# Kernel tuning notes

Hardware: AMD Instinct MI355X
Metric: run time of the kernel (lower is better)

## Reference

```python
import jax, jax.numpy as jnp
import numpy as np

EPS = 1e-12  # matches torch F.normalize eps


def _l2_normalize(x, axis):
    n = jnp.sqrt(jnp.sum(x * x, axis=axis, keepdims=True))
    return x / jnp.maximum(n, EPS)


def setup_inputs() -> dict:
    key = jax.random.key(0)
    k1, k2 = jax.random.split(key)
    phi = jax.random.normal(k1, (64, 512), dtype=jnp.float32)          # (m, H)
    psi = jax.random.normal(k2, (64, 1024, 512), dtype=jnp.float32)    # (m, n, W)
    return {"phi": phi, "psi": psi}


def reference(phi, psi):
    phi = phi.astype(jnp.float32)
    psi = psi.astype(jnp.float32)
    m, H = phi.shape
    m2, n, W = psi.shape
    phi = _l2_normalize(phi, axis=1)   # rows of phi
    psi = _l2_normalize(psi, axis=2)   # each measurement vector

    g_phi_sq = jnp.square(phi @ phi.T)  # (m, m)

    # b[i, j] = sum_{u,v} (psi[i,u] . psi[j,v])^2 = ||psi_i psi_j^T||_F^2
    #         = <psi_i^T psi_i, psi_j^T psi_j>_F  (exact identity, avoids (m,m,n,n))
    S = jnp.einsum('inw,inv->iwv', psi, psi)   # (m, W, W) per-block Gram
    b = jnp.einsum('iwv,jwv->ij', S, S)        # (m, m)

    loss = jnp.sum(g_phi_sq * b) - jnp.float32(m * n)
    return loss
```

## Files before the change

### kernel.cpp

```cpp
#include <hip/hip_runtime.h>
#include <hip/hip_bf16.h>

typedef unsigned short u16;
typedef unsigned int u32;
typedef __attribute__((ext_vector_type(8))) short short8x;
typedef __attribute__((ext_vector_type(4))) float f32x4;

__device__ __forceinline__ u16 bf16u(float x) {
    __hip_bfloat16 h = __float2bfloat16(x);
    return *reinterpret_cast<u16*>(&h);
}

__device__ __forceinline__ void gload_lds16(const void* g, void* l) {
    __builtin_amdgcn_global_load_lds(
        (const __attribute__((address_space(1))) u32*)g,
        (__attribute__((address_space(3))) u32*)l, 16, 0, 0);
}

#define M_  64
#define N_  1024
#define W_  512
#define SP_ROW 163840

__global__ __launch_bounds__(256) void psinorm_t(const float* __restrict__ psi,
                                                 const float* __restrict__ phi,
                                                 u16* __restrict__ psiT,
                                                 float* __restrict__ g2,
                                                 float* __restrict__ out) {
    const int t = threadIdx.x;
    __shared__ u32 tile[64][257];
    __shared__ float djs[4][64], nsqs[64];

    if (blockIdx.x < 1024) {
        const int i  = blockIdx.x >> 4;
        const int nb = blockIdx.x & 15;
        const float* base = psi + ((size_t)i * N_ + (size_t)nb * 64) * W_;
        const int sub = t & 15;

#pragma unroll
        for (int pp = 0; pp < 4; ++pp) {
            const int r = pp * 16 + (t >> 4);
            const float4* rb = (const float4*)(base + (size_t)r * W_) + sub;
            float4 v[8];
            float s = 0.f;
#pragma unroll
            for (int k = 0; k < 8; ++k) {
                v[k] = rb[k * 16];
                s += v[k].x * v[k].x + v[k].y * v[k].y + v[k].z * v[k].z + v[k].w * v[k].w;
            }
#pragma unroll
            for (int o = 1; o < 16; o <<= 1) s += __shfl_xor(s, o);
            const float inv = 1.0f / fmaxf(sqrtf(s), 1e-12f);
#pragma unroll
            for (int k = 0; k < 8; ++k) {
                u32 p0 = (u32)bf16u(v[k].x * inv) | ((u32)bf16u(v[k].y * inv) << 16);
                u32 p1 = (u32)bf16u(v[k].z * inv) | ((u32)bf16u(v[k].w * inv) << 16);
                const int wh = sub * 2 + k * 32;
                tile[r][wh]     = p0;
                tile[r][wh + 1] = p1;
            }
        }
        __syncthreads();

        const u16* t16 = (const u16*)&tile[0][0];
        const int lane = t & 63, wv = t >> 6;
        const int q  = lane & 31;
        const int l5 = lane >> 5;
        u32* out32 = (u32*)psiT + (size_t)i * (W_ * N_ / 2) + nb * 32;
#pragma unroll 4
        for (int it = 0; it < 64; ++it) {
            const int w = it * 8 + wv * 2 + l5;
            u32 lo = (u32)t16[(2 * q)     * 514 + w];
            u32 hi = (u32)t16[(2 * q + 1) * 514 + w];
            out32[(size_t)w * 512 + q] = lo | (hi << 16);
        }
    } else {
        const int gb = blockIdx.x - 1024;
        const int i0 = gb * 4;
        const int lane = t & 63, wv = t >> 6;
        float* pis = (float*)&tile[0][0];
#pragma unroll
        for (int r = 0; r < 4; ++r) {
            pis[r * 512 + t]       = phi[(i0 + r) * 512 + t];
            pis[r * 512 + 256 + t] = phi[(i0 + r) * 512 + 256 + t];
        }
        __syncthreads();

        for (int jj = 0; jj < 16; ++jj) {
            int j = wv + jj * 4;
            const float* pj = phi + j * 512;
            float nn = 0.f, d0 = 0.f, d1 = 0.f, d2 = 0.f, d3 = 0.f;
#pragma unroll
            for (int e = 0; e < 8; ++e) {
                float x = pj[lane + e * 64];
                nn += x * x;
                d0 += pis[0 * 512 + lane + e * 64] * x;
                d1 += pis[1 * 512 + lane + e * 64] * x;
                d2 += pis[2 * 512 + lane + e * 64] * x;
                d3 += pis[3 * 512 + lane + e * 64] * x;
            }
#pragma unroll
            for (int o = 32; o; o >>= 1) {
                nn += __shfl_xor(nn, o);
                d0 += __shfl_xor(d0, o);
                d1 += __shfl_xor(d1, o);
                d2 += __shfl_xor(d2, o);
                d3 += __shfl_xor(d3, o);
            }
            if (lane == 0) {
                djs[0][j] = d0; djs[1][j] = d1; djs[2][j] = d2; djs[3][j] = d3;
                nsqs[j] = nn;
            }
        }
        __syncthreads();
        if (t < 64) {
            const int j = t;
            const float invj = 1.0f / fmaxf(sqrtf(nsqs[j]), 1e-12f);
#pragma unroll
            for (int r = 0; r < 4; ++r) {
                const float invi = 1.0f / fmaxf(sqrtf(nsqs[i0 + r]), 1e-12f);
                const float g = djs[r][j] * invi * invj;
                g2[(i0 + r) * 64 + j] = g * g;
            }
        }
        if (gb == 0 && t == 0) out[0] = -65536.0f;
    }
}

__global__ __launch_bounds__(256) void syrk_bf16(const u16* __restrict__ psiT,
                                                 u16* __restrict__ Sp) {
    const int L = blockIdx.x;
    const int q = L >> 3;
    const int i  = (L & 7) * 8 + q / 10;
    const int bt = q % 10;
    int tr, tc;
    if      (bt < 4) { tr = 0; tc = bt;     }
    else if (bt < 7) { tr = 1; tc = bt - 3; }
    else if (bt < 9) { tr = 2; tc = bt - 5; }
    else             { tr = 3; tc = 3;      }
    const int t = threadIdx.x;

    const u16* Abase = psiT + (size_t)i * W_ * N_ + (size_t)tr * 128 * N_;
    const u16* Bbase = psiT + (size_t)i * W_ * N_ + (size_t)tc * 128 * N_;

    __shared__ alignas(16) u16 ldsA[2][128][64];
    __shared__ alignas(16) u16 ldsB[2][128][64];

    const int lane = t & 63, wv = t >> 6;
    const int wr = wv >> 1, wc = wv & 1;
    const int lrow = lane & 15, lk8 = lane >> 4;

    auto STAGE = [&](int buf, int kt) {
        const int k0 = kt * 64;
#pragma unroll
        for (int r = 0; r < 4; ++r) {
            int c = r * 256 + t;
            int row = c >> 3, cch = c & 7;
            int scch = cch ^ (row & 7);
            gload_lds16(Abase + (size_t)row * N_ + k0 + scch * 8, &ldsA[buf][row][cch * 8]);
            gload_lds16(Bbase + (size_t)row * N_ + k0 + scch * 8, &ldsB[buf][row][cch * 8]);
        }
    };

    f32x4 acc[4][4];
#pragma unroll
    for (int a = 0; a < 4; ++a)
#pragma unroll
        for (int b = 0; b < 4; ++b) acc[a][b] = (f32x4){0.f, 0.f, 0.f, 0.f};

    STAGE(0, 0);
    asm volatile("s_waitcnt vmcnt(0)" ::: "memory");
    __builtin_amdgcn_s_barrier();

    int cur = 0;
    for (int kt = 0; kt < 16; ++kt) {
        if (kt < 15) STAGE(cur ^ 1, kt + 1);
#pragma unroll
        for (int ks = 0; ks < 2; ++ks) {
            short8x af[4], bf[4];
#pragma unroll
            for (int mf = 0; mf < 4; ++mf) {
                int row = wr * 64 + mf * 16 + lrow;
                int ch = (ks * 4 + lk8) ^ (row & 7);
                af[mf] = *(const short8x*)&ldsA[cur][row][ch * 8];
            }
#pragma unroll
            for (int nf = 0; nf < 4; ++nf) {
                int row = wc * 64 + nf * 16 + lrow;
                int ch = (ks * 4 + lk8) ^ (row & 7);
                bf[nf] = *(const short8x*)&ldsB[cur][row][ch * 8];
            }
#pragma unroll
            for (int mf = 0; mf < 4; ++mf)
#pragma unroll
                for (int nf = 0; nf < 4; ++nf)
                    acc[mf][nf] = __builtin_amdgcn_mfma_f32_16x16x32_bf16(
                        af[mf], bf[nf], acc[mf][nf], 0, 0, 0);
        }
        asm volatile("s_waitcnt vmcnt(0)" ::: "memory");
        __builtin_amdgcn_sched_barrier(0);
        __builtin_amdgcn_s_barrier();
        cur ^= 1;
    }

    const float sc = (tr == tc) ? 1.0f : 1.41421356237f;
    size_t Sbase = (size_t)i * SP_ROW + (size_t)bt * 16384;
#pragma unroll
    for (int mf = 0; mf < 4; ++mf)
#pragma unroll
        for (int nf = 0; nf < 4; ++nf)
#pragma unroll
            for (int reg = 0; reg < 4; ++reg) {
                int wl = wr * 64 + mf * 16 + lk8 * 4 + reg;
                int vl = wc * 64 + nf * 16 + lrow;
                Sp[Sbase + (size_t)wl * 128 + vl] = bf16u(acc[mf][nf][reg] * sc);
            }
}

__global__ __launch_bounds__(256) void bgemm_w(const u16* __restrict__ Sp,
                                               const float* __restrict__ g2,
                                               float* __restrict__ out) {
    const int t = threadIdx.x;
    const int lane = t & 63, wv = t >> 6;
    const int wr = wv >> 1, wc = wv & 1;
    const int lrow = lane & 15, lk8 = lane >> 4;
    const size_t kc0 = (size_t)blockIdx.x * 256;

    f32x4 acc[2][2];
#pragma unroll
    for (int a = 0; a < 2; ++a)
#pragma unroll
        for (int b = 0; b < 2; ++b) acc[a][b] = (f32x4){0.f, 0.f, 0.f, 0.f};

#pragma unroll
    for (int ks = 0; ks < 8; ++ks) {
        short8x af[2], bf[2];
#pragma unroll
        for (int mf = 0; mf < 2; ++mf) {
            int row = wr * 32 + mf * 16 + lrow;
            af[mf] = *(const short8x*)(Sp + (size_t)row * SP_ROW + kc0 + (ks * 4 + lk8) * 8);
        }
#pragma unroll
        for (int nf = 0; nf < 2; ++nf) {
            int row = wc * 32 + nf * 16 + lrow;
            bf[nf] = *(const short8x*)(Sp + (size_t)row * SP_ROW + kc0 + (ks * 4 + lk8) * 8);
        }
#pragma unroll
        for (int mf = 0; mf < 2; ++mf)
#pragma unroll
            for (int nf = 0; nf < 2; ++nf)
                acc[mf][nf] = __builtin_amdgcn_mfma_f32_16x16x32_bf16(
                    af[mf], bf[nf], acc[mf][nf], 0, 0, 0);
    }

    float wsum = 0.f;
#pragma unroll
    for (int mf = 0; mf < 2; ++mf)
#pragma unroll
        for (int nf = 0; nf < 2; ++nf) {
            const int jc = wc * 32 + nf * 16 + lrow;
#pragma unroll
            for (int reg = 0; reg < 4; ++reg) {
                const int ir = wr * 32 + mf * 16 + lk8 * 4 + reg;
                wsum += acc[mf][nf][reg] * g2[ir * 64 + jc];
            }
        }
#pragma unroll
    for (int o = 32; o; o >>= 1) wsum += __shfl_down(wsum, o);
    __shared__ float w4[4];
    if (lane == 0) w4[wv] = wsum;
    __syncthreads();
    if (t == 0) atomicAdd(out, w4[0] + w4[1] + w4[2] + w4[3]);
}

__global__ void wsfail(float* __restrict__ out) {
    if (threadIdx.x == 0) out[0] = 1.0e30f;
}

extern "C" void kernel_launch(void* const* d_in, const int* in_sizes, int n_in,
                              void* d_out, int out_size, void* d_ws, size_t ws_size,
                              hipStream_t stream) {
    const float* phi = (const float*)d_in[0];
    const float* psi = (const float*)d_in[1];
    float* out = (float*)d_out;
    char* ws = (char*)d_ws;

    const size_t NEEDED = 67108864ull + 20971520ull + 16384ull;
    if (ws_size < NEEDED) {
        wsfail<<<1, 64, 0, stream>>>(out);
        return;
    }
    u16*   psiT = (u16*)(ws);
    u16*   Sp   = (u16*)(ws + 67108864);
    float* g2   = (float*)(ws + 88080384);

    psinorm_t<<<1040, 256, 0, stream>>>(psi, phi, psiT, g2, out);
    syrk_bf16<<<640,  256, 0, stream>>>(psiT, Sp);
    bgemm_w  <<<640,  256, 0, stream>>>(Sp, g2, out);
}
```

Before: 268.8 us.

## Split psi normalization and bf16 transpose into separate norm and transpose kernels

The fused normalize-and-transpose kernel is split into two. The first computes per-row inverse norms and the phi Gram, and the second rereads psi in 64-column strips, scales it, converts it to bf16 and writes the transposed layout. The intent is better-coalesced transpose writes: each wave now writes 512-byte contiguous runs instead of 128-byte fragments. The cost is reading the 128MB psi input twice plus an extra kernel launch.

```diff
diff --git a/kernel.cpp b/kernel.cpp
--- a/kernel.cpp
+++ b/kernel.cpp
@@ -22,70 +22,45 @@
 #define W_  512
 #define SP_ROW 163840
 
-__global__ __launch_bounds__(256) void psinorm_t(const float* __restrict__ psi,
-                                                 const float* __restrict__ phi,
-                                                 u16* __restrict__ psiT,
-                                                 float* __restrict__ g2,
-                                                 float* __restrict__ out) {
+__global__ __launch_bounds__(256) void p0_norms(const float* __restrict__ psi,
+                                                const float* __restrict__ phi,
+                                                float* __restrict__ invs,
+                                                float* __restrict__ g2,
+                                                float* __restrict__ out) {
     const int t = threadIdx.x;
-    __shared__ u32 tile[64][257];
+    __shared__ float pis[2048];
     __shared__ float djs[4][64], nsqs[64];
 
     if (blockIdx.x < 1024) {
         const int i  = blockIdx.x >> 4;
         const int nb = blockIdx.x & 15;
+        const int sub = t & 15;
         const float* base = psi + ((size_t)i * N_ + (size_t)nb * 64) * W_;
-        const int sub = t & 15;
-
 #pragma unroll
         for (int pp = 0; pp < 4; ++pp) {
             const int r = pp * 16 + (t >> 4);
             const float4* rb = (const float4*)(base + (size_t)r * W_) + sub;
-            float4 v[8];
             float s = 0.f;
 #pragma unroll
             for (int k = 0; k < 8; ++k) {
-                v[k] = rb[k * 16];
-                s += v[k].x * v[k].x + v[k].y * v[k].y + v[k].z * v[k].z + v[k].w * v[k].w;
+                float4 v = rb[k * 16];
+                s += v.x * v.x + v.y * v.y + v.z * v.z + v.w * v.w;
             }
 #pragma unroll
             for (int o = 1; o < 16; o <<= 1) s += __shfl_xor(s, o);
-            const float inv = 1.0f / fmaxf(sqrtf(s), 1e-12f);
-#pragma unroll
-            for (int k = 0; k < 8; ++k) {
-                u32 p0 = (u32)bf16u(v[k].x * inv) | ((u32)bf16u(v[k].y * inv) << 16);
-                u32 p1 = (u32)bf16u(v[k].z * inv) | ((u32)bf16u(v[k].w * inv) << 16);
-                const int wh = sub * 2 + k * 32;
-                tile[r][wh]     = p0;
-                tile[r][wh + 1] = p1;
-            }
-        }
-        __syncthreads();
-
-        const u16* t16 = (const u16*)&tile[0][0];
-        const int lane = t & 63, wv = t >> 6;
-        const int q  = lane & 31;
-        const int l5 = lane >> 5;
-        u32* out32 = (u32*)psiT + (size_t)i * (W_ * N_ / 2) + nb * 32;
-#pragma unroll 4
-        for (int it = 0; it < 64; ++it) {
-            const int w = it * 8 + wv * 2 + l5;
-            u32 lo = (u32)t16[(2 * q)     * 514 + w];
-            u32 hi = (u32)t16[(2 * q + 1) * 514 + w];
-            out32[(size_t)w * 512 + q] = lo | (hi << 16);
+            if (sub == 0)
+                invs[i * N_ + nb * 64 + r] = 1.0f / fmaxf(sqrtf(s), 1e-12f);
         }
     } else {
         const int gb = blockIdx.x - 1024;
         const int i0 = gb * 4;
         const int lane = t & 63, wv = t >> 6;
-        float* pis = (float*)&tile[0][0];
 #pragma unroll
         for (int r = 0; r < 4; ++r) {
             pis[r * 512 + t]       = phi[(i0 + r) * 512 + t];
             pis[r * 512 + 256 + t] = phi[(i0 + r) * 512 + 256 + t];
         }
         __syncthreads();
-
         for (int jj = 0; jj < 16; ++jj) {
             int j = wv + jj * 4;
             const float* pj = phi + j * 512;
@@ -124,6 +99,53 @@
             }
         }
         if (gb == 0 && t == 0) out[0] = -65536.0f;
+    }
+}
+
+__global__ __launch_bounds__(256) void p1_transpose(const float* __restrict__ psi,
+                                                    const float* __restrict__ invs,
+                                                    u16* __restrict__ psiT) {
+    const int t  = threadIdx.x;
+    const int i  = blockIdx.x >> 3;
+    const int wc = blockIdx.x & 7;
+    const int w0 = wc * 64;
+
+    __shared__ u16   tile[64][258];
+    __shared__ float invl[1024];
+
+    ((float4*)invl)[t] = ((const float4*)(invs + (size_t)i * N_))[t];
+
+    const int sub = t & 15;
+    const int rr  = t >> 4;
+    const float* base = psi + (size_t)i * N_ * W_ + w0;
+    u32* out32 = (u32*)psiT + (size_t)i * (W_ * N_ / 2);
+    const int lane = t & 63, wv = t >> 6;
+
+    for (int s = 0; s < 4; ++s) {
+        const int nbase = s * 256;
+        __syncthreads();
+#pragma unroll
+        for (int rnd = 0; rnd < 16; ++rnd) {
+            const int n = rnd * 16 + rr;
+            float4 v = *(const float4*)(base + (size_t)(nbase + n) * W_ + sub * 4);
+            const float inv = invl[nbase + n];
+            const int wl = sub * 4;
+            tile[wl + 0][n] = bf16u(v.x * inv);
+            tile[wl + 1][n] = bf16u(v.y * inv);
+            tile[wl + 2][n] = bf16u(v.z * inv);
+            tile[wl + 3][n] = bf16u(v.w * inv);
+        }
+        __syncthreads();
+#pragma unroll
+        for (int ww = 0; ww < 16; ++ww) {
+            const int w = wv * 16 + ww;
+#pragma unroll
+            for (int h = 0; h < 2; ++h) {
+                const int c = h * 64 + lane;
+                u32 val = *(const u32*)&tile[w][2 * c];
+                out32[(size_t)(w0 + w) * 512 + (nbase >> 1) + c] = val;
+            }
+        }
     }
 }
 
@@ -285,7 +307,7 @@
     float* out = (float*)d_out;
     char* ws = (char*)d_ws;
 
-    const size_t NEEDED = 67108864ull + 20971520ull + 16384ull;
+    const size_t NEEDED = 67108864ull + 20971520ull + 16384ull + 262144ull;
     if (ws_size < NEEDED) {
         wsfail<<<1, 64, 0, stream>>>(out);
         return;
@@ -293,8 +315,10 @@
     u16*   psiT = (u16*)(ws);
     u16*   Sp   = (u16*)(ws + 67108864);
     float* g2   = (float*)(ws + 88080384);
-
-    psinorm_t<<<1040, 256, 0, stream>>>(psi, phi, psiT, g2, out);
-    syrk_bf16<<<640,  256, 0, stream>>>(psiT, Sp);
-    bgemm_w  <<<640,  256, 0, stream>>>(Sp, g2, out);
-}
+    float* invs = (float*)(ws + 88096768);
+
+    p0_norms    <<<1040, 256, 0, stream>>>(psi, phi, invs, g2, out);
+    p1_transpose<<<512,  256, 0, stream>>>(psi, invs, psiT);
+    syrk_bf16   <<<640,  256, 0, stream>>>(psiT, Sp);
+    bgemm_w     <<<640,  256, 0, stream>>>(Sp, g2, out);
+}
```

Result: slower. 285.1 us (+6.1%).
